# Kernel tuning notes

Hardware: AMD Instinct MI355X
Metric: run time of the kernel (lower is better)

The kernel has to match this reference:

```python
import jax, jax.numpy as jnp
import numpy as np

N = 100_000      # nodes
E = 1_600_000    # edges (avg degree 16)
B = 50           # graphs in batch
GSIZE = N // B   # nodes per graph
IN = 128
HID = 128
NC = 10
K = 2


def setup_inputs() -> dict:
    key = jax.random.key(0)
    ks = jax.random.split(key, 10)
    # edges kept within each graph so the batched readout is realistic
    g = jax.random.randint(ks[0], (E,), 0, B)
    src = (g * GSIZE + jax.random.randint(ks[1], (E,), 0, GSIZE)).astype(jnp.int32)
    dst = (g * GSIZE + jax.random.randint(ks[2], (E,), 0, GSIZE)).astype(jnp.int32)
    graph_ids = (jnp.arange(N) // GSIZE).astype(jnp.int32)
    x = jax.random.normal(ks[3], (N, IN), jnp.float32)
    s1 = 1.0 / np.sqrt(K * IN)
    s2 = 1.0 / np.sqrt(K * HID)
    sc = 1.0 / np.sqrt(HID)
    W1 = jax.random.normal(ks[4], (K * IN, HID), jnp.float32) * s1
    b1 = jnp.zeros((HID,), jnp.float32)
    W2 = jax.random.normal(ks[5], (K * HID, HID), jnp.float32) * s2
    b2 = jnp.zeros((HID,), jnp.float32)
    Wc = jax.random.normal(ks[6], (HID, NC), jnp.float32) * sc
    bc = jnp.zeros((NC,), jnp.float32)
    return dict(x=x, W1=W1, b1=b1, W2=W2, b2=b2, Wc=Wc, bc=bc,
                src=src, dst=dst, graph_ids=graph_ids)


def _spmm_norm(feat, src, dst, dinv):
    # D^{-1/2} A D^{-1/2} feat  (copy_u + sum over in-edges)
    m = (feat * dinv)[src]                                    # [E, D]
    agg = jax.ops.segment_sum(m, dst, num_segments=N)         # [N, D]
    return agg * dinv


def _cheb_conv(feat, src, dst, dinv, W, b):
    # lambda_max = 2 -> re_norm = 1, L_hat = -D^{-1/2} A D^{-1/2}
    Tx0 = feat
    Tx1 = -_spmm_norm(feat, src, dst, dinv)                   # k=2 Cheb recursion
    h = jnp.concatenate([Tx0, Tx1], axis=-1) @ W + b          # DGL Linear(k*in, out)
    return jax.nn.relu(h)


def reference(x, W1, b1, W2, b2, Wc, bc, src, dst, graph_ids):
    deg = jax.ops.segment_sum(jnp.ones((E,), jnp.float32), dst, num_segments=N)
    dinv = jnp.clip(deg, 1.0, None) ** -0.5                   # in-degree^{-1/2}
    dinv = dinv[:, None]
    h = _cheb_conv(x, src, dst, dinv, W1, b1)                 # [N, HID]
    h = _cheb_conv(h, src, dst, dinv, W2, b2)                 # [N, HID]
    hg = jax.ops.segment_max(h, graph_ids, num_segments=B)    # MaxPooling readout [B, HID]
    return hg @ Wc + bc                                       # [B, NC]
```

## Files before the change

kernel.cpp:

```cpp
#include <hip/hip_runtime.h>

#define N_NODES 100000
#define N_EDGES 1600000
#define NB      50
#define GSIZE   2000
#define FEAT    128
#define NC      10
#define NSB     400
#define BCAP    5120
#define CHUNK   2048
#define NBLK_A  782

using short8 = __attribute__((ext_vector_type(8))) short;
using f32x4  = __attribute__((ext_vector_type(4))) float;

__device__ __forceinline__ unsigned bf16rnd(float f) {
    unsigned u = __float_as_uint(f);
    return (u + 0x7fffu + ((u >> 16) & 1u)) >> 16;
}
__device__ __forceinline__ float blo(unsigned w) { return __uint_as_float(w << 16); }
__device__ __forceinline__ float bhi(unsigned w) { return __uint_as_float(w & 0xffff0000u); }

__device__ __forceinline__ void gload_lds16(const void* g, void* l) {
    __builtin_amdgcn_global_load_lds(
        (const __attribute__((address_space(1))) unsigned int*)g,
        (__attribute__((address_space(3))) unsigned int*)l, 16, 0, 0);
}

__device__ __forceinline__ int graph_of(int k, int gi) {
    if (gi < 6) return k + 8 * gi;
    return (k < 2) ? (48 + k) : -1;
}

__global__ __launch_bounds__(256) void k_binA(
    const int* __restrict__ src, const int* __restrict__ dst,
    unsigned* __restrict__ gbuf, int* __restrict__ gcur) {
    __shared__ int cnt[NSB];
    __shared__ int base[NSB];
    __shared__ int gbase[NSB];
    __shared__ int tsum[256];
    __shared__ unsigned stage[CHUNK];
    __shared__ unsigned short bslot[CHUNK];
    __shared__ int total_s;
    int tid = threadIdx.x;
    int e0 = blockIdx.x * CHUNK;
    for (int i = tid; i < NSB; i += 256) cnt[i] = 0;
    __syncthreads();

    unsigned pv[8]; int pb[8], pr[8];
#pragma unroll
    for (int q = 0; q < 8; ++q) {
        int e = e0 + q * 256 + tid;
        pb[q] = -1;
        if (e < N_EDGES) {
            int d = dst[e];
            int g = d / 2000;
            int l = d - g * 2000;
            int sb = g * 8 + l / 250;
            pv[q] = ((unsigned)src[e] << 11) | (unsigned)l;
            pb[q] = sb;
            pr[q] = atomicAdd(&cnt[sb], 1);
        }
    }
    __syncthreads();
    int v0 = (2 * tid     < NSB) ? cnt[2 * tid]     : 0;
    int v1 = (2 * tid + 1 < NSB) ? cnt[2 * tid + 1] : 0;
    int loc = v0 + v1;
    tsum[tid] = loc; __syncthreads();
    for (int off = 1; off < 256; off <<= 1) {
        int t = (tid >= off) ? tsum[tid - off] : 0;
        __syncthreads(); tsum[tid] += t; __syncthreads();
    }
    int pref = tsum[tid] - loc;
    if (2 * tid     < NSB) base[2 * tid]     = pref;
    if (2 * tid + 1 < NSB) base[2 * tid + 1] = pref + v0;
    if (tid == 255) total_s = tsum[255];
    __syncthreads();
#pragma unroll
    for (int q = 0; q < 8; ++q) {
        if (pb[q] >= 0) {
            int s = base[pb[q]] + pr[q];
            stage[s] = pv[q];
            bslot[s] = (unsigned short)pb[q];
        }
    }
    for (int b = tid; b < NSB; b += 256) gbase[b] = atomicAdd(&gcur[b], cnt[b]);
    __syncthreads();
    int total = total_s;
    for (int s = tid; s < total; s += 256) {
        int b = bslot[s];
        gbuf[(size_t)b * BCAP + gbase[b] + (s - base[b])] = stage[s];
    }
}

__global__ __launch_bounds__(256) void k_prepB(
    const unsigned* __restrict__ gbuf, const int* __restrict__ gcur,
    const float* __restrict__ x,
    int* __restrict__ rowstart, float* __restrict__ dinv, float* __restrict__ sdeg,
    int* __restrict__ csrc, ushort* __restrict__ Yh) {
    __shared__ int hist[256];
    __shared__ int tsum[256];
    __shared__ int lcur[256];
    __shared__ float dvs[256];
    __shared__ int stage[BCAP];
    __shared__ int base_s;
    int B = blockIdx.x; int k = B & 7, j = B >> 3;
    int gi = j >> 3, q = j & 7;
    int g = graph_of(k, gi);
    if (g < 0) return;
    int tid = threadIdx.x;
    int sb = g * 8 + q;
    int n0l = q * 250;
    hist[tid] = 0;
    int acc = 0;
    for (int i = tid; i < sb; i += 256) acc += gcur[i];
    tsum[tid] = acc;
    __syncthreads();
    for (int off = 128; off > 0; off >>= 1) {
        if (tid < off) tsum[tid] += tsum[tid + off];
        __syncthreads();
    }
    if (tid == 0) base_s = tsum[0];
    int nq = gcur[sb];
    const unsigned* bp = gbuf + (size_t)sb * BCAP;
    for (int i = tid; i < nq; i += 256)
        atomicAdd(&hist[(int)(bp[i] & 2047u) - n0l], 1);
    __syncthreads();
    int base = base_s;
    int v = hist[tid];
    tsum[tid] = v; __syncthreads();
    for (int off = 1; off < 256; off <<= 1) {
        int t = (tid >= off) ? tsum[tid - off] : 0;
        __syncthreads(); tsum[tid] += t; __syncthreads();
    }
    int pref = tsum[tid] - v;
    lcur[tid] = pref;
    if (tid < 250) {
        int node = g * GSIZE + n0l + tid;
        rowstart[node] = base + pref;
        float d = fmaxf((float)v, 1.f);
        float dv = rsqrtf(d);
        dinv[node] = dv;
        dvs[tid] = dv;
        sdeg[node] = sqrtf(d);
    }
    if (g == 49 && q == 7 && tid == 0) rowstart[N_NODES] = base + nq;
    __syncthreads();
    for (int i = tid; i < nq; i += 256) {
        unsigned w = bp[i];
        int d = (int)(w & 2047u) - n0l;
        int p = atomicAdd(&lcur[d], 1);
        stage[p] = (int)(w >> 11);
    }
    __syncthreads();
    for (int s = tid; s < nq; s += 256)
        csrc[base + s] = stage[s];

    const float4* x4 = (const float4*)x;
    uint2* Y2 = (uint2*)Yh;
    int nodebase = g * GSIZE + n0l;
#pragma unroll 4
    for (int idx = tid; idx < 250 * 32; idx += 256) {
        int r = idx >> 5, cc = idx & 31;
        float dv = dvs[r];
        float4 vx = x4[(size_t)(nodebase + r) * 32 + cc];
        uint2 yo;
        yo.x = bf16rnd(vx.x * dv) | (bf16rnd(vx.y * dv) << 16);
        yo.y = bf16rnd(vx.z * dv) | (bf16rnd(vx.w * dv) << 16);
        Y2[(size_t)(nodebase + r) * 32 + cc] = yo;
    }
}

__global__ void k_packW(const float* __restrict__ W1, const float* __restrict__ W2,
                        ushort* __restrict__ W1h, ushort* __restrict__ W1l,
                        ushort* __restrict__ W2h, ushort* __restrict__ W2l) {
    int b = blockIdx.x;
    const float* W = (b < 128) ? W1 : W2;
    ushort* Wh = (b < 128) ? W1h : W2h;
    ushort* Wl = (b < 128) ? W1l : W2l;
    int idx = (b & 127) * 256 + threadIdx.x;
    int j = idx & 7, l = (idx >> 3) & 63, kb = (idx >> 9) & 7, c = idx >> 12;
    int k = kb * 32 + (l >> 4) * 8 + j;
    int col = c * 16 + (l & 15);
    float w = W[k * 128 + col];
    unsigned h = bf16rnd(w);
    float rem = w - __uint_as_float(h << 16);
    Wh[idx] = (ushort)h;
    Wl[idx] = (ushort)bf16rnd(rem);
}

__device__ __forceinline__ void acc8(float* a, uint4 u) {
    a[0] += blo(u.x); a[1] += bhi(u.x); a[2] += blo(u.y); a[3] += bhi(u.y);
    a[4] += blo(u.z); a[5] += bhi(u.z); a[6] += blo(u.w); a[7] += bhi(u.w);
}
__global__ __launch_bounds__(256) void k_gather(
    const ushort* __restrict__ Yh, const float* __restrict__ dinv,
    const int* __restrict__ rowstart, const int* __restrict__ csrc,
    ushort* __restrict__ Th) {
    int B = blockIdx.x; int k = B & 7, j = B >> 3;
    int gi = j / 125, local = j % 125;
    int g = graph_of(k, gi);
    if (g < 0) return;
    int tid = threadIdx.x;
    int c = tid & 15;
    int i = tid >> 4;
    int n = g * GSIZE + local * 16 + i;
    int rs = rowstart[n], re = rowstart[n + 1];
    float dn = -dinv[n];
    const uint4* Y4 = (const uint4*)Yh;
    float a0[8] = {0.f}, a1[8] = {0.f}, a2[8] = {0.f}, a3[8] = {0.f};
    int e = rs;
    for (; e + 3 < re; e += 4) {
        int s0 = csrc[e], s1 = csrc[e + 1], s2 = csrc[e + 2], s3 = csrc[e + 3];
        uint4 u0 = Y4[s0 * 16 + c];
        uint4 u1 = Y4[s1 * 16 + c];
        uint4 u2 = Y4[s2 * 16 + c];
        uint4 u3 = Y4[s3 * 16 + c];
        acc8(a0, u0); acc8(a1, u1); acc8(a2, u2); acc8(a3, u3);
    }
    if (e < re) {
        bool c1 = e + 1 < re, c2 = e + 2 < re;
        int s0 = csrc[e];
        int s1 = c1 ? csrc[e + 1] : s0;
        int s2 = c2 ? csrc[e + 2] : s0;
        uint4 u0 = Y4[s0 * 16 + c];
        uint4 u1 = Y4[s1 * 16 + c];
        uint4 u2 = Y4[s2 * 16 + c];
        if (!c1) { u1.x = 0u; u1.y = 0u; u1.z = 0u; u1.w = 0u; }
        if (!c2) { u2.x = 0u; u2.y = 0u; u2.z = 0u; u2.w = 0u; }
        acc8(a0, u0); acc8(a1, u1); acc8(a2, u2);
    }
#pragma unroll
    for (int t = 0; t < 8; ++t) a0[t] = (a0[t] + a1[t]) + (a2[t] + a3[t]);
    uint4 o;
    o.x = bf16rnd(a0[0] * dn) | (bf16rnd(a0[1] * dn) << 16);
    o.y = bf16rnd(a0[2] * dn) | (bf16rnd(a0[3] * dn) << 16);
    o.z = bf16rnd(a0[4] * dn) | (bf16rnd(a0[5] * dn) << 16);
    o.w = bf16rnd(a0[6] * dn) | (bf16rnd(a0[7] * dn) << 16);
    ((uint4*)Th)[n * 16 + c] = o;
}

__global__ __launch_bounds__(256, 4) void k_gemm(
    const ushort* __restrict__ Yh, const ushort* __restrict__ Th,
    const ushort* __restrict__ Wh, const ushort* __restrict__ Wl,
    const float* __restrict__ bias, const float* __restrict__ dinv,
    const float* __restrict__ sdeg,
    ushort* __restrict__ Oy, float* __restrict__ hg, int mode) {
    __shared__ uint4 ldsY[1280];
    __shared__ uint4 ldsT[1280];
    int B = blockIdx.x; int k = B & 7, j = B >> 3;
    int gi = j / 25, local = j % 25;
    int g = graph_of(k, gi);
    if (g < 0) return;
    int tid = threadIdx.x;
    int lane = tid & 63, wave = tid >> 6;
    int m = lane & 15, quad = lane >> 4;
    int rowbase = g * GSIZE + local * 80;

    const uint4* Y4 = (const uint4*)Yh;
    const uint4* T4 = (const uint4*)Th;
#pragma unroll
    for (int it = 0; it < 5; ++it) {
        int ci = it * 256 + tid;
        int lr = ci >> 4, cc = ci & 15;
        int sc = cc ^ (lr & 7);
        size_t go = (size_t)(rowbase + lr) * 16 + sc;
        gload_lds16(Y4 + go, &ldsY[it * 256 + wave * 64]);
        gload_lds16(T4 + go, &ldsT[it * 256 + wave * 64]);
    }
    __syncthreads();

#pragma unroll 1
    for (int ci2 = 0; ci2 < 2; ++ci2) {
        int c = wave + ci2 * 4;
        int colc = c * 16 + m;
        float bb = bias[colc];

        f32x4 accA[5], accB[5];
#pragma unroll
        for (int rt = 0; rt < 5; ++rt) {
            accA[rt] = (f32x4){0.f, 0.f, 0.f, 0.f};
            accB[rt] = (f32x4){0.f, 0.f, 0.f, 0.f};
        }

#pragma unroll 1
        for (int kb = 0; kb < 4; ++kb) {
            int boA = ((c * 8 + kb) * 64 + lane) * 8;
            int boB = ((c * 8 + kb + 4) * 64 + lane) * 8;
            short8 whA = *reinterpret_cast<const short8*>(Wh + boA);
            short8 wlA = *reinterpret_cast<const short8*>(Wl + boA);
            short8 whB = *reinterpret_cast<const short8*>(Wh + boB);
            short8 wlB = *reinterpret_cast<const short8*>(Wl + boB);
            int qq = (kb * 4 + quad) ^ (m & 7);
#pragma unroll
            for (int rt = 0; rt < 5; ++rt) {
                int lr = rt * 16 + m;
                short8 aY = *reinterpret_cast<const short8*>(&ldsY[(lr << 4) | qq]);
                short8 aT = *reinterpret_cast<const short8*>(&ldsT[(lr << 4) | qq]);
                accA[rt] = __builtin_amdgcn_mfma_f32_16x16x32_bf16(aY, whA, accA[rt], 0, 0, 0);
                accA[rt] = __builtin_amdgcn_mfma_f32_16x16x32_bf16(aY, wlA, accA[rt], 0, 0, 0);
                accB[rt] = __builtin_amdgcn_mfma_f32_16x16x32_bf16(aT, whB, accB[rt], 0, 0, 0);
                accB[rt] = __builtin_amdgcn_mfma_f32_16x16x32_bf16(aT, wlB, accB[rt], 0, 0, 0);
            }
        }

        if (mode == 0) {
#pragma unroll
            for (int rt = 0; rt < 5; ++rt) {
#pragma unroll
                for (int r = 0; r < 4; ++r) {
                    int orow = rowbase + rt * 16 + quad * 4 + r;
                    float s = sdeg[orow], dv = dinv[orow];
                    float v = fmaxf(accA[rt][r] * s + accB[rt][r] + bb, 0.f);
                    Oy[orow * FEAT + colc] = (ushort)bf16rnd(v * dv);
                }
            }
        } else {
            float runc = 0.f;
#pragma unroll
            for (int rt = 0; rt < 5; ++rt) {
#pragma unroll
                for (int r = 0; r < 4; ++r) {
                    float s = sdeg[rowbase + rt * 16 + quad * 4 + r];
                    runc = fmaxf(runc, fmaxf(accA[rt][r] * s + accB[rt][r] + bb, 0.f));
                }
            }
            runc = fmaxf(runc, __shfl_xor(runc, 16));
            runc = fmaxf(runc, __shfl_xor(runc, 32));
            if (lane < 16) {
                atomicMax((int*)&hg[g * FEAT + colc], __float_as_int(runc));
            }
        }
    }
}

__global__ void k_classify(const float* __restrict__ hg, const float* __restrict__ Wc,
                           const float* __restrict__ bc, float* __restrict__ out) {
    int g = blockIdx.x, t = threadIdx.x;
    if (t < NC) {
        float acc = bc[t];
        for (int j = 0; j < FEAT; ++j) acc += hg[g * FEAT + j] * Wc[j * NC + t];
        out[g * NC + t] = acc;
    }
}

extern "C" void kernel_launch(void* const* d_in, const int* in_sizes, int n_in,
                              void* d_out, int out_size, void* d_ws, size_t ws_size,
                              hipStream_t stream) {
    const float* x   = (const float*)d_in[0];
    const float* W1  = (const float*)d_in[1];
    const float* b1  = (const float*)d_in[2];
    const float* W2  = (const float*)d_in[3];
    const float* b2  = (const float*)d_in[4];
    const float* Wc  = (const float*)d_in[5];
    const float* bc  = (const float*)d_in[6];
    const int*   src = (const int*)d_in[7];
    const int*   dst = (const int*)d_in[8];
    float* out = (float*)d_out;

    char* ws = (char*)d_ws;
    size_t off = 0;
    auto alloc = [&](size_t bytes) { char* p = ws + off; off += (bytes + 255) & ~(size_t)255; return p; };
    int*      gcur     = (int*)     alloc(NSB * 4);
    float*    hg       = (float*)   alloc(NB * FEAT * 4);
    float*    dinv     = (float*)   alloc(N_NODES * 4);
    float*    sdeg     = (float*)   alloc(N_NODES * 4);
    int*      rowstart = (int*)     alloc((N_NODES + 1) * 4);
    unsigned* gbuf     = (unsigned*)alloc((size_t)NSB * BCAP * 4);
    int*      csrc     = (int*)     alloc((size_t)N_EDGES * 4);
    ushort*   W1h      = (ushort*)  alloc(256 * 128 * 2);
    ushort*   W1l      = (ushort*)  alloc(256 * 128 * 2);
    ushort*   W2h      = (ushort*)  alloc(256 * 128 * 2);
    ushort*   W2l      = (ushort*)  alloc(256 * 128 * 2);
    ushort*   Yh       = (ushort*)  alloc((size_t)N_NODES * FEAT * 2);
    ushort*   Y2h      = (ushort*)  alloc((size_t)N_NODES * FEAT * 2);
    ushort*   Th       = (ushort*)  alloc((size_t)N_NODES * FEAT * 2);

    hipMemsetAsync(gcur, 0, 1792 + NB * FEAT * 4, stream);

    k_binA<<<NBLK_A, 256, 0, stream>>>(src, dst, gbuf, gcur);
    k_prepB<<<448, 256, 0, stream>>>(gbuf, gcur, x, rowstart, dinv, sdeg, csrc, Yh);

    k_packW<<<256, 256, 0, stream>>>(W1, W2, W1h, W1l, W2h, W2l);

    k_gather<<<7000, 256, 0, stream>>>(Yh, dinv, rowstart, csrc, Th);
    k_gemm<<<1400, 256, 0, stream>>>(Yh, Th, W1h, W1l, b1, dinv, sdeg, Y2h, nullptr, 0);
    k_gather<<<7000, 256, 0, stream>>>(Y2h, dinv, rowstart, csrc, Th);
    k_gemm<<<1400, 256, 0, stream>>>(Y2h, Th, W2h, W2l, b2, dinv, sdeg, nullptr, hg, 1);

    k_classify<<<NB, 64, 0, stream>>>(hg, Wc, bc, out);
}
```

Before: 271.8 us.

## Fuse weight packing into edge binning kernel and enlarge binning chunks

```diff
diff --git a/kernel.cpp b/kernel.cpp
--- a/kernel.cpp
+++ b/kernel.cpp
@@ -8,8 +8,8 @@
 #define NC      10
 #define NSB     400
 #define BCAP    5120
-#define CHUNK   2048
-#define NBLK_A  782
+#define CHUNK   8192
+#define NBLK_A  196
 
 using short8 = __attribute__((ext_vector_type(8))) short;
 using f32x4  = __attribute__((ext_vector_type(4))) float;
@@ -32,9 +32,28 @@
     return (k < 2) ? (48 + k) : -1;
 }
 
-__global__ __launch_bounds__(256) void k_binA(
+__global__ __launch_bounds__(256) void k_binAW(
     const int* __restrict__ src, const int* __restrict__ dst,
-    unsigned* __restrict__ gbuf, int* __restrict__ gcur) {
+    const float* __restrict__ W1, const float* __restrict__ W2,
+    unsigned* __restrict__ gbuf, int* __restrict__ gcur,
+    ushort* __restrict__ W1h, ushort* __restrict__ W1l,
+    ushort* __restrict__ W2h, ushort* __restrict__ W2l) {
+    if (blockIdx.x >= NBLK_A) {
+        int b = blockIdx.x - NBLK_A;
+        const float* W = (b < 128) ? W1 : W2;
+        ushort* Wh = (b < 128) ? W1h : W2h;
+        ushort* Wl = (b < 128) ? W1l : W2l;
+        int idx = (b & 127) * 256 + threadIdx.x;
+        int j = idx & 7, l = (idx >> 3) & 63, kb = (idx >> 9) & 7, c = idx >> 12;
+        int k = kb * 32 + (l >> 4) * 8 + j;
+        int col = c * 16 + (l & 15);
+        float w = W[k * 128 + col];
+        unsigned h = bf16rnd(w);
+        float rem = w - __uint_as_float(h << 16);
+        Wh[idx] = (ushort)h;
+        Wl[idx] = (ushort)bf16rnd(rem);
+        return;
+    }
     __shared__ int cnt[NSB];
     __shared__ int base[NSB];
     __shared__ int gbase[NSB];
@@ -47,19 +66,15 @@
     for (int i = tid; i < NSB; i += 256) cnt[i] = 0;
     __syncthreads();
 
-    unsigned pv[8]; int pb[8], pr[8];
-#pragma unroll
-    for (int q = 0; q < 8; ++q) {
+#pragma unroll 4
+    for (int q = 0; q < 32; ++q) {
         int e = e0 + q * 256 + tid;
-        pb[q] = -1;
         if (e < N_EDGES) {
             int d = dst[e];
             int g = d / 2000;
             int l = d - g * 2000;
             int sb = g * 8 + l / 250;
-            pv[q] = ((unsigned)src[e] << 11) | (unsigned)l;
-            pb[q] = sb;
-            pr[q] = atomicAdd(&cnt[sb], 1);
+            atomicAdd(&cnt[sb], 1);
         }
     }
     __syncthreads();
@@ -76,15 +91,25 @@
     if (2 * tid + 1 < NSB) base[2 * tid + 1] = pref + v0;
     if (tid == 255) total_s = tsum[255];
     __syncthreads();
-#pragma unroll
-    for (int q = 0; q < 8; ++q) {
-        if (pb[q] >= 0) {
-            int s = base[pb[q]] + pr[q];
-            stage[s] = pv[q];
-            bslot[s] = (unsigned short)pb[q];
-        }
-    }
-    for (int b = tid; b < NSB; b += 256) gbase[b] = atomicAdd(&gcur[b], cnt[b]);
+    for (int b = tid; b < NSB; b += 256) {
+        int c = cnt[b];
+        gbase[b] = atomicAdd(&gcur[b], c);
+        cnt[b] = base[b];
+    }
+    __syncthreads();
+#pragma unroll 4
+    for (int q = 0; q < 32; ++q) {
+        int e = e0 + q * 256 + tid;
+        if (e < N_EDGES) {
+            int d = dst[e];
+            int g = d / 2000;
+            int l = d - g * 2000;
+            int sb = g * 8 + l / 250;
+            int p = atomicAdd(&cnt[sb], 1);
+            stage[p] = ((unsigned)src[e] << 11) | (unsigned)l;
+            bslot[p] = (unsigned short)sb;
+        }
+    }
     __syncthreads();
     int total = total_s;
     for (int s = tid; s < total; s += 256) {
@@ -169,24 +194,6 @@
         yo.y = bf16rnd(vx.z * dv) | (bf16rnd(vx.w * dv) << 16);
         Y2[(size_t)(nodebase + r) * 32 + cc] = yo;
     }
-}
-
-__global__ void k_packW(const float* __restrict__ W1, const float* __restrict__ W2,
-                        ushort* __restrict__ W1h, ushort* __restrict__ W1l,
-                        ushort* __restrict__ W2h, ushort* __restrict__ W2l) {
-    int b = blockIdx.x;
-    const float* W = (b < 128) ? W1 : W2;
-    ushort* Wh = (b < 128) ? W1h : W2h;
-    ushort* Wl = (b < 128) ? W1l : W2l;
-    int idx = (b & 127) * 256 + threadIdx.x;
-    int j = idx & 7, l = (idx >> 3) & 63, kb = (idx >> 9) & 7, c = idx >> 12;
-    int k = kb * 32 + (l >> 4) * 8 + j;
-    int col = c * 16 + (l & 15);
-    float w = W[k * 128 + col];
-    unsigned h = bf16rnd(w);
-    float rem = w - __uint_as_float(h << 16);
-    Wh[idx] = (ushort)h;
-    Wl[idx] = (ushort)bf16rnd(rem);
 }
 
 __device__ __forceinline__ void acc8(float* a, uint4 u) {
@@ -378,10 +385,9 @@
 
     hipMemsetAsync(gcur, 0, 1792 + NB * FEAT * 4, stream);
 
-    k_binA<<<NBLK_A, 256, 0, stream>>>(src, dst, gbuf, gcur);
+    k_binAW<<<NBLK_A + 256, 256, 0, stream>>>(src, dst, W1, W2, gbuf, gcur,
+                                              W1h, W1l, W2h, W2l);
     k_prepB<<<448, 256, 0, stream>>>(gbuf, gcur, x, rowstart, dinv, sdeg, csrc, Yh);
-
-    k_packW<<<256, 256, 0, stream>>>(W1, W2, W1h, W1l, W2h, W2l);
 
     k_gather<<<7000, 256, 0, stream>>>(Yh, dinv, rowstart, csrc, Th);
     k_gemm<<<1400, 256, 0, stream>>>(Yh, Th, W1h, W1l, b1, dinv, sdeg, Y2h, nullptr, 0);
```

Result: slower. 277.3 us (+2.0%).
